# Optimization experiments

Hardware: AMD Instinct MI355X
Metric: run time of the kernel (lower is better)

Reference implementation:

```python
import jax, jax.numpy as jnp
import numpy as np
import math

D = 1024
H = 16
DH = D // H
FF = 4096
B, S = 2, 2048


def _layernorm(x, g, b, eps=1e-5):
    mu = jnp.mean(x, axis=-1, keepdims=True)
    var = jnp.var(x, axis=-1, keepdims=True)
    return (x - mu) * jax.lax.rsqrt(var + eps) * g + b


def _gelu_tanh(x):
    # 0.5*x*(1+tanh(sqrt(2/pi)*(x+0.044715*x^3)))
    c = math.sqrt(2.0 / math.pi)
    return 0.5 * x * (1.0 + jnp.tanh(c * (x + 0.044715 * x ** 3)))


def setup_inputs() -> dict:
    key = jax.random.key(0)
    ks = jax.random.split(key, 8)
    s = 0.02
    return {
        "x": jax.random.normal(ks[0], (B, S, D), dtype=jnp.float32),
        "ln1_g": jnp.ones((D,), jnp.float32),
        "ln1_b": jnp.zeros((D,), jnp.float32),
        "Wqkv": jax.random.normal(ks[1], (D, 3 * D), jnp.float32) * s,
        "bqkv": jnp.zeros((3 * D,), jnp.float32),
        "Wo": jax.random.normal(ks[2], (D, D), jnp.float32) * s,
        "bo": jnp.zeros((D,), jnp.float32),
        "ln2_g": jnp.ones((D,), jnp.float32),
        "ln2_b": jnp.zeros((D,), jnp.float32),
        "W1": jax.random.normal(ks[3], (D, FF), jnp.float32) * s,
        "b1": jnp.zeros((FF,), jnp.float32),
        "W2": jax.random.normal(ks[4], (FF, D), jnp.float32) * s,
        "b2": jnp.zeros((D,), jnp.float32),
    }


def reference(x, ln1_g, ln1_b, Wqkv, bqkv, Wo, bo, ln2_g, ln2_b, W1, b1, W2, b2):
    b, s, d = x.shape
    h = _layernorm(x, ln1_g, ln1_b)
    qkv = h @ Wqkv + bqkv                       # [B,S,3D]
    q, k, v = jnp.split(qkv, 3, axis=-1)
    q = q.reshape(b, s, H, DH).transpose(0, 2, 1, 3)   # [B,H,S,Dh]
    k = k.reshape(b, s, H, DH).transpose(0, 2, 1, 3)
    v = v.reshape(b, s, H, DH).transpose(0, 2, 1, 3)
    scores = jnp.einsum("bhqd,bhkd->bhqk", q, k) / math.sqrt(DH)
    probs = jax.nn.softmax(scores, axis=-1)
    attn = jnp.einsum("bhqk,bhkd->bhqd", probs, v)     # [B,H,S,Dh]
    attn = attn.transpose(0, 2, 1, 3).reshape(b, s, d)
    attn = attn @ Wo + bo
    x = x + attn
    m = _layernorm(x, ln2_g, ln2_b)
    m = _gelu_tanh(m @ W1 + b1) @ W2 + b2
    return x + m
```

## Files before the change

kernel.cpp:

```cpp
#include <hip/hip_runtime.h>
#include <hip/hip_bf16.h>
#include <cstdint>

#define D_ 1024
#define H_ 16
#define DH_ 64
#define FF_ 4096
#define B_ 2
#define S_ 2048
#define MR_ (B_ * S_)

typedef __bf16 bf16x8 __attribute__((ext_vector_type(8)));
typedef __bf16 bf16x4 __attribute__((ext_vector_type(4)));
typedef float f32x4 __attribute__((ext_vector_type(4)));
typedef float f32x16 __attribute__((ext_vector_type(16)));

__device__ __forceinline__ void g2lds16(const void* g, void* l) {
  __builtin_amdgcn_global_load_lds(
      (__attribute__((address_space(1))) void*)(uintptr_t)g,
      (__attribute__((address_space(3))) void*)(uint32_t)(uintptr_t)l,
      16, 0, 0);
}

__device__ __forceinline__ unsigned pkbf16(float lo, float hi) {
  unsigned r;
  asm("v_cvt_pk_bf16_f32 %0, %1, %2" : "=v"(r) : "v"(lo), "v"(hi));
  return r;
}

__device__ __forceinline__ float max3f(float a, float b, float c) {
  float d;
  asm("v_max3_f32 %0, %1, %2, %3" : "=v"(d) : "v"(a), "v"(b), "v"(c));
  return d;
}

__device__ __forceinline__ float rmax16(const f32x16& v) {
  float t0 = max3f(v[0], v[1], v[2]);
  float t1 = max3f(v[3], v[4], v[5]);
  float t2 = max3f(v[6], v[7], v[8]);
  float t3 = max3f(v[9], v[10], v[11]);
  float t4 = max3f(v[12], v[13], v[14]);
  return fmaxf(max3f(t0, t1, t2), max3f(t3, t4, v[15]));
}

__global__ __launch_bounds__(256) void transpose_cvt(
    const float* __restrict__ W, __hip_bfloat16* __restrict__ Wt, int K, int N) {
  __shared__ float t[32][33];
  int bx = blockIdx.x * 32;
  int by = blockIdx.y * 32;
  int tx = threadIdx.x, ty = threadIdx.y;
#pragma unroll
  for (int i = 0; i < 4; ++i)
    t[ty + 8 * i][tx] = W[(size_t)(by + ty + 8 * i) * N + bx + tx];
  __syncthreads();
#pragma unroll
  for (int i = 0; i < 4; ++i)
    Wt[(size_t)(bx + ty + 8 * i) * K + by + tx] = __float2bfloat16(t[tx][ty + 8 * i]);
}

__global__ __launch_bounds__(256) void transpose_v(
    const __hip_bfloat16* __restrict__ qkv, __hip_bfloat16* __restrict__ vT) {
  __shared__ __hip_bfloat16 t[32][33];
  int bh = blockIdx.z, b = bh >> 4, h = bh & 15;
  int s0 = blockIdx.x * 32, d0 = blockIdx.y * 32;
  int tx = threadIdx.x, ty = threadIdx.y;
#pragma unroll
  for (int i = 0; i < 4; ++i)
    t[ty + 8 * i][tx] =
        qkv[(size_t)(b * S_ + s0 + ty + 8 * i) * (3 * D_) + 2 * D_ + h * DH_ + d0 + tx];
  __syncthreads();
#pragma unroll
  for (int i = 0; i < 4; ++i)
    vT[(size_t)(bh * DH_ + d0 + ty + 8 * i) * S_ + s0 + tx] = t[tx][ty + 8 * i];
}

__global__ __launch_bounds__(256) void ln_kernel(
    const float* __restrict__ x, const float* __restrict__ g,
    const float* __restrict__ b, __hip_bfloat16* __restrict__ out) {
  int row = blockIdx.x;
  const float4* xr = (const float4*)(x + (size_t)row * D_);
  float4 v = xr[threadIdx.x];
  float s = v.x + v.y + v.z + v.w;
  float ss = v.x * v.x + v.y * v.y + v.z * v.z + v.w * v.w;
#pragma unroll
  for (int m = 1; m < 64; m <<= 1) {
    s += __shfl_xor(s, m);
    ss += __shfl_xor(ss, m);
  }
  __shared__ float rs[4], rss[4];
  int wave = threadIdx.x >> 6, lane = threadIdx.x & 63;
  if (lane == 0) { rs[wave] = s; rss[wave] = ss; }
  __syncthreads();
  s = rs[0] + rs[1] + rs[2] + rs[3];
  ss = rss[0] + rss[1] + rss[2] + rss[3];
  float mean = s * (1.0f / D_);
  float var = ss * (1.0f / D_) - mean * mean;
  float inv = rsqrtf(var + 1e-5f);
  int c = threadIdx.x * 4;
  float4 gv = ((const float4*)g)[threadIdx.x];
  float4 bv = ((const float4*)b)[threadIdx.x];
  __hip_bfloat16* o = out + (size_t)row * D_ + c;
  o[0] = __float2bfloat16((v.x - mean) * inv * gv.x + bv.x);
  o[1] = __float2bfloat16((v.y - mean) * inv * gv.y + bv.y);
  o[2] = __float2bfloat16((v.z - mean) * inv * gv.z + bv.z);
  o[3] = __float2bfloat16((v.w - mean) * inv * gv.w + bv.w);
}

template <int EPI, int BM, int WM, int WN>
__global__ __launch_bounds__(512) void gemm3(
    const __hip_bfloat16* __restrict__ A, const __hip_bfloat16* __restrict__ Bt,
    const float* __restrict__ bias, const float* __restrict__ resid,
    void* __restrict__ outp, int M, int N, int K) {
  constexpr int BN = 128;
  constexpr int MF = BM / (WM * 16);
  constexpr int NF = BN / (WN * 16);
  constexpr int VMN = BM / 64 + 2;
  __shared__ alignas(16) __hip_bfloat16 sA[3][BM * 64];
  __shared__ alignas(16) __hip_bfloat16 sB[3][BN * 64];
  const int tid = threadIdx.x;
  const int lane = tid & 63, wave = tid >> 6;
  const int l15 = lane & 15, l4 = lane >> 4;
  const int wr = wave / WN, wc = wave % WN;
  const int csw = (l15 & 7) << 3;

  const int gx = gridDim.x;
  int nwg = gx * gridDim.y;
  int flat = blockIdx.y * gx + blockIdx.x;
  int cpx = nwg >> 3;
  int swz = (flat & 7) * cpx + (flat >> 3);
  const int m0 = (swz / gx) * BM, n0 = (swz % gx) * BN;

  f32x4 z = {0.f, 0.f, 0.f, 0.f};
  f32x4 acc[MF][NF];
#pragma unroll
  for (int i = 0; i < MF; ++i)
#pragma unroll
    for (int j = 0; j < NF; ++j) acc[i][j] = z;

  auto stageA = [&](int bu, int kt) {
#pragma unroll
    for (int it = 0; it < BM / 64; ++it) {
      int idx = it * 512 + tid;
      int r = idx >> 3, c = (idx & 7) * 8;
      int cs = c ^ ((r & 7) << 3);
      g2lds16(A + (size_t)(m0 + r) * K + kt + cs, (void*)(&sA[bu][idx * 8]));
    }
  };
  auto stageB = [&](int bu, int kt) {
#pragma unroll
    for (int it = 0; it < 2; ++it) {
      int idx = it * 512 + tid;
      int r = idx >> 3, c = (idx & 7) * 8;
      int cs = c ^ ((r & 7) << 3);
      g2lds16(Bt + (size_t)(n0 + r) * K + kt + cs, (void*)(&sB[bu][idx * 8]));
    }
  };

  const int nk = K / 64;
  stageA(0, 0);
  stageB(0, 0);
  stageA(1, 64);
  stageB(1, 64);
  if constexpr (VMN == 6)
    asm volatile("s_waitcnt vmcnt(6)" ::: "memory");
  else
    asm volatile("s_waitcnt vmcnt(4)" ::: "memory");
  __builtin_amdgcn_s_barrier();

  int bu = 0, bu2 = 2;
  for (int j = 0; j < nk; ++j) {
    const bool pf = (j + 2) < nk;
    if (pf) stageA(bu2, (j + 2) * 64);

    __builtin_amdgcn_s_setprio(1);
#pragma unroll
    for (int kk = 0; kk < 2; ++kk) {
      bf16x8 bfr[NF];
      int col = (kk * 32 + l4 * 8) ^ csw;
#pragma unroll
      for (int nf = 0; nf < NF; ++nf)
        bfr[nf] = *(const bf16x8*)(&sB[bu][(wc * NF * 16 + nf * 16 + l15) * 64 + col]);
#pragma unroll
      for (int mf = 0; mf < MF; ++mf) {
        bf16x8 af = *(const bf16x8*)(&sA[bu][(wr * MF * 16 + mf * 16 + l15) * 64 + col]);
#pragma unroll
        for (int nf = 0; nf < NF; ++nf)
          acc[mf][nf] =
              __builtin_amdgcn_mfma_f32_16x16x32_bf16(af, bfr[nf], acc[mf][nf], 0, 0, 0);
      }
    }
    __builtin_amdgcn_s_setprio(0);

    if (pf) stageB(bu2, (j + 2) * 64);

    asm volatile("s_waitcnt lgkmcnt(0)" ::: "memory");
    __builtin_amdgcn_sched_barrier(0);

    if (pf) {
      if constexpr (VMN == 6)
        asm volatile("s_waitcnt vmcnt(6)" ::: "memory");
      else
        asm volatile("s_waitcnt vmcnt(4)" ::: "memory");
    } else {
      asm volatile("s_waitcnt vmcnt(0)" ::: "memory");
    }
    __builtin_amdgcn_s_barrier();
    asm volatile("" ::: "memory");
    bu = (bu == 2) ? 0 : bu + 1;
    bu2 = (bu2 == 2) ? 0 : bu2 + 1;
  }

#pragma unroll
  for (int mf = 0; mf < MF; ++mf) {
#pragma unroll
    for (int nf = 0; nf < NF; ++nf) {
      int col = n0 + wc * NF * 16 + nf * 16 + l15;
      float bv = bias[col];
#pragma unroll
      for (int j = 0; j < 4; ++j) {
        int row = m0 + wr * MF * 16 + mf * 16 + l4 * 4 + j;
        size_t o = (size_t)row * N + col;
        float v = acc[mf][nf][j] + bv;
        if (EPI == 0) {
          ((__hip_bfloat16*)outp)[o] = __float2bfloat16(v);
        } else if (EPI == 1) {
          ((float*)outp)[o] = v + resid[o];
        } else {
          float a = 0.7978845608028654f * (v + 0.044715f * v * v * v);
          a = fminf(fmaxf(a, -15.f), 15.f);
          float e = __expf(2.f * a);
          float th = (e - 1.f) / (e + 1.f);
          ((__hip_bfloat16*)outp)[o] = __float2bfloat16(0.5f * v * (1.f + th));
        }
      }
    }
  }
}

__global__ __launch_bounds__(256) void attn_kernel(
    const __hip_bfloat16* __restrict__ qkv, const __hip_bfloat16* __restrict__ vT,
    __hip_bfloat16* __restrict__ out) {
  __shared__ alignas(16) __hip_bfloat16 sK[2][64 * 64];
  __shared__ alignas(16) __hip_bfloat16 sV[2][64 * 64];
  __shared__ float sBr[4][32];
  const int tid = threadIdx.x, lane = tid & 63, wave = tid >> 6;
  const int l31 = lane & 31, hi = lane >> 5;
  const int bh = blockIdx.y, b = bh >> 4, h = bh & 15;
  const int q0 = blockIdx.x * 128;
  const int rsw = (l31 & 7) << 3;
  const float k2 = 0.125f * 1.44269504f;

  bf16x8 qf[4];
  {
    int qr = q0 + wave * 32 + l31;
    const size_t qbase = ((size_t)(b * S_ + qr)) * (3 * D_) + h * DH_;
#pragma unroll
    for (int ks = 0; ks < 4; ++ks) {
      bf16x8 q = *(const bf16x8*)(qkv + qbase + ks * 16 + hi * 8);
#pragma unroll
      for (int i = 0; i < 8; ++i) q[i] = (__bf16)((float)q[i] * k2);
      qf[ks] = q;
    }
  }

  bf16x8 onesb;
#pragma unroll
  for (int i = 0; i < 8; ++i) onesb[i] = (__bf16)1.0f;

  f32x16 acc0, acc1, accL;
#pragma unroll
  for (int r = 0; r < 16; ++r) { acc0[r] = 0.f; acc1[r] = 0.f; accL[r] = 0.f; }
  float mrun = -1e30f;

  const __hip_bfloat16* kg = qkv + (size_t)b * S_ * (3 * D_) + D_ + h * DH_;
  const __hip_bfloat16* vg = vT + (size_t)bh * DH_ * S_;

  auto stage = [&](int bu, int kv0) {
#pragma unroll
    for (int it = 0; it < 2; ++it) {
      int idx = it * 256 + tid;
      int r = idx >> 3;
      int c = (idx & 7) * 8;
      int cs = c ^ ((r & 7) << 3);
      g2lds16(kg + (size_t)(kv0 + r) * (3 * D_) + cs, (void*)(&sK[bu][idx * 8]));
      g2lds16(vg + (size_t)r * S_ + kv0 + cs, (void*)(&sV[bu][idx * 8]));
    }
  };

  stage(0, 0);
  const int NT = S_ / 64;

  for (int t = 0; t < NT; ++t) {
    const int cur = t & 1;
    __syncthreads();
    if (t + 1 < NT) stage(cur ^ 1, (t + 1) * 64);

    f32x16 sf0, sf1;
#pragma unroll
    for (int r = 0; r < 16; ++r) { sf0[r] = 0.f; sf1[r] = 0.f; }
    __builtin_amdgcn_s_setprio(1);
#pragma unroll
    for (int ks = 0; ks < 4; ++ks) {
      int colsw = (ks * 16 + hi * 8) ^ rsw;
      bf16x8 kf0 = *(const bf16x8*)(&sK[cur][l31 * 64 + colsw]);
      bf16x8 kf1 = *(const bf16x8*)(&sK[cur][(32 + l31) * 64 + colsw]);
      sf0 = __builtin_amdgcn_mfma_f32_32x32x16_bf16(kf0, qf[ks], sf0, 0, 0, 0);
      sf1 = __builtin_amdgcn_mfma_f32_32x32x16_bf16(kf1, qf[ks], sf1, 0, 0, 0);
    }
    __builtin_amdgcn_s_setprio(0);

    float pm = fmaxf(rmax16(sf0), rmax16(sf1));
    if (!__all(pm - mrun <= 8.0f)) {
      float mf = fmaxf(pm, __shfl_xor(pm, 32));
      float mn = fmaxf(mrun, mf);
      float corrl = exp2f(mrun - mn);
      mrun = mn;
      sBr[wave][l31] = corrl;
#pragma unroll
      for (int r = 0; r < 16; ++r) {
        float cr = sBr[wave][(r & 3) + 8 * (r >> 2) + 4 * hi];
        acc0[r] *= cr;
        acc1[r] *= cr;
        accL[r] *= cr;
      }
    }

    bf16x8 pa[4];
#pragma unroll
    for (int kb = 0; kb < 2; ++kb) {
      const f32x16 s16 = kb ? sf1 : sf0;
#pragma unroll
      for (int ksb = 0; ksb < 2; ++ksb) {
        float p0 = exp2f(s16[8 * ksb + 0] - mrun);
        float p1 = exp2f(s16[8 * ksb + 1] - mrun);
        float p2 = exp2f(s16[8 * ksb + 2] - mrun);
        float p3 = exp2f(s16[8 * ksb + 3] - mrun);
        float p4 = exp2f(s16[8 * ksb + 4] - mrun);
        float p5 = exp2f(s16[8 * ksb + 5] - mrun);
        float p6 = exp2f(s16[8 * ksb + 6] - mrun);
        float p7 = exp2f(s16[8 * ksb + 7] - mrun);
        unsigned wa = pkbf16(p0, p1), wb = pkbf16(p2, p3);
        unsigned wc = pkbf16(p4, p5), wd = pkbf16(p6, p7);
        auto r1 = __builtin_amdgcn_permlane32_swap(wa, wc, false, false);
        auto r2 = __builtin_amdgcn_permlane32_swap(wb, wd, false, false);
        union { unsigned u[4]; bf16x8 v; } w;
        w.u[0] = r1[0]; w.u[1] = r2[0]; w.u[2] = r1[1]; w.u[3] = r2[1];
        pa[kb * 2 + ksb] = w.v;
      }
    }

    __builtin_amdgcn_s_setprio(1);
#pragma unroll
    for (int ksg = 0; ksg < 4; ++ksg) {
      int colsw = (ksg * 16 + hi * 8) ^ rsw;
      bf16x8 vf0 = *(const bf16x8*)(&sV[cur][l31 * 64 + colsw]);
      bf16x8 vf1 = *(const bf16x8*)(&sV[cur][(32 + l31) * 64 + colsw]);
      acc0 = __builtin_amdgcn_mfma_f32_32x32x16_bf16(pa[ksg], vf0, acc0, 0, 0, 0);
      acc1 = __builtin_amdgcn_mfma_f32_32x32x16_bf16(pa[ksg], vf1, acc1, 0, 0, 0);
      accL = __builtin_amdgcn_mfma_f32_32x32x16_bf16(pa[ksg], onesb, accL, 0, 0, 0);
    }
    __builtin_amdgcn_s_setprio(0);
  }

#pragma unroll
  for (int r = 0; r < 16; ++r) {
    int qrow = (r & 3) + 8 * (r >> 2) + 4 * hi;
    float ir = 1.0f / accL[r];
    size_t obase = ((size_t)(b * S_ + q0 + wave * 32 + qrow)) * D_ + h * DH_ + l31;
    out[obase] = __float2bfloat16(acc0[r] * ir);
    out[obase + 32] = __float2bfloat16(acc1[r] * ir);
  }
}

extern "C" void kernel_launch(void* const* d_in, const int* in_sizes, int n_in,
                              void* d_out, int out_size, void* d_ws, size_t ws_size,
                              hipStream_t stream) {
  const float* x = (const float*)d_in[0];
  const float* ln1_g = (const float*)d_in[1];
  const float* ln1_b = (const float*)d_in[2];
  const float* Wqkv = (const float*)d_in[3];
  const float* bqkv = (const float*)d_in[4];
  const float* Wo = (const float*)d_in[5];
  const float* bo = (const float*)d_in[6];
  const float* ln2_g = (const float*)d_in[7];
  const float* ln2_b = (const float*)d_in[8];
  const float* W1 = (const float*)d_in[9];
  const float* b1 = (const float*)d_in[10];
  const float* W2 = (const float*)d_in[11];
  const float* b2 = (const float*)d_in[12];
  float* out = (float*)d_out;

  char* ws = (char*)d_ws;
  size_t off = 0;
  auto alloc = [&](size_t bytes) {
    void* p = ws + off;
    off += (bytes + 255) & ~(size_t)255;
    return p;
  };
  __hip_bfloat16* WqkvT = (__hip_bfloat16*)alloc((size_t)3 * D_ * D_ * 2);
  __hip_bfloat16* WoT = (__hip_bfloat16*)alloc((size_t)D_ * D_ * 2);
  __hip_bfloat16* W1T = (__hip_bfloat16*)alloc((size_t)FF_ * D_ * 2);
  __hip_bfloat16* W2T = (__hip_bfloat16*)alloc((size_t)D_ * FF_ * 2);
  __hip_bfloat16* h = (__hip_bfloat16*)alloc((size_t)MR_ * D_ * 2);
  __hip_bfloat16* qkv = (__hip_bfloat16*)alloc((size_t)MR_ * FF_ * 2);
  __hip_bfloat16* ff = qkv;
  __hip_bfloat16* vT = (__hip_bfloat16*)alloc((size_t)B_ * H_ * DH_ * S_ * 2);
  __hip_bfloat16* attn_out = (__hip_bfloat16*)alloc((size_t)MR_ * D_ * 2);

  dim3 tb(32, 8);
  transpose_cvt<<<dim3(3 * D_ / 32, D_ / 32), tb, 0, stream>>>(Wqkv, WqkvT, D_, 3 * D_);
  transpose_cvt<<<dim3(D_ / 32, D_ / 32), tb, 0, stream>>>(Wo, WoT, D_, D_);
  transpose_cvt<<<dim3(FF_ / 32, D_ / 32), tb, 0, stream>>>(W1, W1T, D_, FF_);
  transpose_cvt<<<dim3(D_ / 32, FF_ / 32), tb, 0, stream>>>(W2, W2T, FF_, D_);
  ln_kernel<<<MR_, 256, 0, stream>>>(x, ln1_g, ln1_b, h);
  gemm3<0, 128, 2, 4><<<dim3(3 * D_ / 128, MR_ / 128), 512, 0, stream>>>(
      h, WqkvT, bqkv, nullptr, qkv, MR_, 3 * D_, D_);
  transpose_v<<<dim3(S_ / 32, DH_ / 32, B_ * H_), tb, 0, stream>>>(qkv, vT);
  attn_kernel<<<dim3(S_ / 128, B_ * H_), 256, 0, stream>>>(qkv, vT, attn_out);
  gemm3<1, 128, 2, 4><<<dim3(D_ / 128, MR_ / 128), 512, 0, stream>>>(
      attn_out, WoT, bo, x, out, MR_, D_, D_);
  ln_kernel<<<MR_, 256, 0, stream>>>(out, ln2_g, ln2_b, h);
  gemm3<2, 256, 4, 2><<<dim3(FF_ / 128, MR_ / 256), 512, 0, stream>>>(
      h, W1T, b1, nullptr, ff, MR_, FF_, D_);
  gemm3<1, 128, 2, 4><<<dim3(D_ / 128, MR_ / 128), 512, 0, stream>>>(
      ff, W2T, b2, out, out, MR_, D_, FF_);
}
```

Before: 239.7 us.

## Simplify GEMM to double-buffered single-stage prefetch with fixed 128x128 tiles

Replaces the three-buffer LDS pipeline (prefetching two k-steps ahead, with A and B loads split around the MFMA block) with a two-buffer scheme that prefetches one step ahead and waits for all loads each iteration. It also removes the BM/warp-layout template parameters, so the W1 GEMM now uses 128x128 tiles instead of 256x128. This reduces LDS usage and code complexity. The cost is less latency hiding and more A/B tile traffic for the FFN up-projection.

```diff
diff --git a/kernel.cpp b/kernel.cpp
--- a/kernel.cpp
+++ b/kernel.cpp
@@ -106,17 +106,14 @@
   o[3] = __float2bfloat16((v.w - mean) * inv * gv.w + bv.w);
 }
 
-template <int EPI, int BM, int WM, int WN>
+template <int EPI>
 __global__ __launch_bounds__(512) void gemm3(
     const __hip_bfloat16* __restrict__ A, const __hip_bfloat16* __restrict__ Bt,
     const float* __restrict__ bias, const float* __restrict__ resid,
     void* __restrict__ outp, int M, int N, int K) {
-  constexpr int BN = 128;
-  constexpr int MF = BM / (WM * 16);
-  constexpr int NF = BN / (WN * 16);
-  constexpr int VMN = BM / 64 + 2;
-  __shared__ alignas(16) __hip_bfloat16 sA[3][BM * 64];
-  __shared__ alignas(16) __hip_bfloat16 sB[3][BN * 64];
+  constexpr int BM = 128, BN = 128, MF = 4, NF = 2, WN = 4;
+  __shared__ alignas(16) __hip_bfloat16 sA[2][BM * 64];
+  __shared__ alignas(16) __hip_bfloat16 sB[2][BN * 64];
   const int tid = threadIdx.x;
   const int lane = tid & 63, wave = tid >> 6;
   const int l15 = lane & 15, l4 = lane >> 4;
@@ -137,40 +134,25 @@
 #pragma unroll
     for (int j = 0; j < NF; ++j) acc[i][j] = z;
 
-  auto stageA = [&](int bu, int kt) {
-#pragma unroll
-    for (int it = 0; it < BM / 64; ++it) {
+  auto stage = [&](int bu, int kt) {
+#pragma unroll
+    for (int it = 0; it < 2; ++it) {
       int idx = it * 512 + tid;
       int r = idx >> 3, c = (idx & 7) * 8;
       int cs = c ^ ((r & 7) << 3);
       g2lds16(A + (size_t)(m0 + r) * K + kt + cs, (void*)(&sA[bu][idx * 8]));
+      g2lds16(Bt + (size_t)(n0 + r) * K + kt + cs, (void*)(&sB[bu][idx * 8]));
     }
   };
-  auto stageB = [&](int bu, int kt) {
-#pragma unroll
-    for (int it = 0; it < 2; ++it) {
-      int idx = it * 512 + tid;
-      int r = idx >> 3, c = (idx & 7) * 8;
-      int cs = c ^ ((r & 7) << 3);
-      g2lds16(Bt + (size_t)(n0 + r) * K + kt + cs, (void*)(&sB[bu][idx * 8]));
-    }
-  };
 
   const int nk = K / 64;
-  stageA(0, 0);
-  stageB(0, 0);
-  stageA(1, 64);
-  stageB(1, 64);
-  if constexpr (VMN == 6)
-    asm volatile("s_waitcnt vmcnt(6)" ::: "memory");
-  else
-    asm volatile("s_waitcnt vmcnt(4)" ::: "memory");
+  stage(0, 0);
+  asm volatile("s_waitcnt vmcnt(0)" ::: "memory");
   __builtin_amdgcn_s_barrier();
 
-  int bu = 0, bu2 = 2;
   for (int j = 0; j < nk; ++j) {
-    const bool pf = (j + 2) < nk;
-    if (pf) stageA(bu2, (j + 2) * 64);
+    const int cur = j & 1;
+    if (j + 1 < nk) stage(cur ^ 1, (j + 1) * 64);
 
     __builtin_amdgcn_s_setprio(1);
 #pragma unroll
@@ -179,10 +161,10 @@
       int col = (kk * 32 + l4 * 8) ^ csw;
 #pragma unroll
       for (int nf = 0; nf < NF; ++nf)
-        bfr[nf] = *(const bf16x8*)(&sB[bu][(wc * NF * 16 + nf * 16 + l15) * 64 + col]);
+        bfr[nf] = *(const bf16x8*)(&sB[cur][(wc * NF * 16 + nf * 16 + l15) * 64 + col]);
 #pragma unroll
       for (int mf = 0; mf < MF; ++mf) {
-        bf16x8 af = *(const bf16x8*)(&sA[bu][(wr * MF * 16 + mf * 16 + l15) * 64 + col]);
+        bf16x8 af = *(const bf16x8*)(&sA[cur][(wr * MF * 16 + mf * 16 + l15) * 64 + col]);
 #pragma unroll
         for (int nf = 0; nf < NF; ++nf)
           acc[mf][nf] =
@@ -191,23 +173,11 @@
     }
     __builtin_amdgcn_s_setprio(0);
 
-    if (pf) stageB(bu2, (j + 2) * 64);
-
     asm volatile("s_waitcnt lgkmcnt(0)" ::: "memory");
     __builtin_amdgcn_sched_barrier(0);
-
-    if (pf) {
-      if constexpr (VMN == 6)
-        asm volatile("s_waitcnt vmcnt(6)" ::: "memory");
-      else
-        asm volatile("s_waitcnt vmcnt(4)" ::: "memory");
-    } else {
-      asm volatile("s_waitcnt vmcnt(0)" ::: "memory");
-    }
+    asm volatile("s_waitcnt vmcnt(0)" ::: "memory");
     __builtin_amdgcn_s_barrier();
     asm volatile("" ::: "memory");
-    bu = (bu == 2) ? 0 : bu + 1;
-    bu2 = (bu2 == 2) ? 0 : bu2 + 1;
   }
 
 #pragma unroll
@@ -413,15 +383,15 @@
   transpose_cvt<<<dim3(FF_ / 32, D_ / 32), tb, 0, stream>>>(W1, W1T, D_, FF_);
   transpose_cvt<<<dim3(D_ / 32, FF_ / 32), tb, 0, stream>>>(W2, W2T, FF_, D_);
   ln_kernel<<<MR_, 256, 0, stream>>>(x, ln1_g, ln1_b, h);
-  gemm3<0, 128, 2, 4><<<dim3(3 * D_ / 128, MR_ / 128), 512, 0, stream>>>(
+  gemm3<0><<<dim3(3 * D_ / 128, MR_ / 128), 512, 0, stream>>>(
       h, WqkvT, bqkv, nullptr, qkv, MR_, 3 * D_, D_);
   transpose_v<<<dim3(S_ / 32, DH_ / 32, B_ * H_), tb, 0, stream>>>(qkv, vT);
   attn_kernel<<<dim3(S_ / 128, B_ * H_), 256, 0, stream>>>(qkv, vT, attn_out);
-  gemm3<1, 128, 2, 4><<<dim3(D_ / 128, MR_ / 128), 512, 0, stream>>>(
+  gemm3<1><<<dim3(D_ / 128, MR_ / 128), 512, 0, stream>>>(
       attn_out, WoT, bo, x, out, MR_, D_, D_);
   ln_kernel<<<MR_, 256, 0, stream>>>(out, ln2_g, ln2_b, h);
-  gemm3<2, 256, 4, 2><<<dim3(FF_ / 128, MR_ / 256), 512, 0, stream>>>(
+  gemm3<2><<<dim3(FF_ / 128, MR_ / 128), 512, 0, stream>>>(
       h, W1T, b1, nullptr, ff, MR_, FF_, D_);
-  gemm3<1, 128, 2, 4><<<dim3(D_ / 128, MR_ / 128), 512, 0, stream>>>(
+  gemm3<1><<<dim3(D_ / 128, MR_ / 128), 512, 0, stream>>>(
       ff, W2T, b2, out, out, MR_, D_, FF_);
 }
```

Result: faster. 234.7 us (-2.1%).
